# Optimization experiments

Hardware: AMD Instinct MI355X
Metric: run time of the kernel (lower is better)

The kernel has to match this reference:

```python
import jax, jax.numpy as jnp
import numpy as np

B, T, D = 4, 2048, 1024
H = 16
HD = D // H
NORM = float(np.sqrt(D))  # module uses sqrt(out_features), not sqrt(head_dim)


def setup_inputs() -> dict:
    key = jax.random.key(0)
    k1, k2, k3 = jax.random.split(key, 3)
    x = jax.random.normal(k1, (B, T, D), dtype=jnp.float32)
    w_qkv = jax.random.normal(k2, (D, 3 * D), dtype=jnp.float32) * (1.0 / np.sqrt(D))
    w_proj = jax.random.normal(k3, (D, D), dtype=jnp.float32) * (1.0 / np.sqrt(D))
    return {"x": x, "w_qkv": w_qkv, "w_proj": w_proj}


def reference(x, w_qkv, w_proj):
    b, t, _ = x.shape
    qkv = jnp.einsum('btd,de->bte', x, w_qkv)  # [B,T,3D]
    q, k, v = jnp.split(qkv, 3, axis=-1)
    # [B,H,T,HD]
    q = q.reshape(b, t, H, HD).transpose(0, 2, 1, 3)
    k = k.reshape(b, t, H, HD).transpose(0, 2, 1, 3)
    v = v.reshape(b, t, H, HD).transpose(0, 2, 1, 3)
    attn = jnp.einsum('bhqd,bhkd->bhqk', q, k) / NORM
    causal = jnp.tril(jnp.ones((t, t), dtype=bool))
    attn = jnp.where(causal[None, None], attn, -jnp.inf)
    attn = jax.nn.softmax(attn, axis=-1)
    y = jnp.einsum('bhqk,bhkd->bhqd', attn, v)
    out = y.transpose(0, 2, 1, 3).reshape(b, t, D)
    return jnp.einsum('btd,de->bte', out, w_proj)
```

## Files before the change

### kernel.cpp

```cpp
#include <hip/hip_runtime.h>
#include <hip/hip_bf16.h>
#include <cstdint>
#include <cstddef>

typedef __bf16 bfx8 __attribute__((ext_vector_type(8)));
typedef float  fx4  __attribute__((ext_vector_type(4)));
typedef float  fx16 __attribute__((ext_vector_type(16)));

#define MFMA_B16(a, b, c)  __builtin_amdgcn_mfma_f32_16x16x32_bf16((a), (b), (c), 0, 0, 0)
#define MFMA32(a, b, c)    __builtin_amdgcn_mfma_f32_32x32x16_bf16((a), (b), (c), 0, 0, 0)

#define GLD_LDS16(gsrc, ldst)                                                  \
  __builtin_amdgcn_global_load_lds(                                            \
      (const __attribute__((address_space(1))) void*)(gsrc),                   \
      (__attribute__((address_space(3))) void*)(ldst), 16, 0, 0)

static __device__ __forceinline__ unsigned short f2bf(float f) {
  union { float f; unsigned u; } v; v.f = f;
  unsigned r = v.u + 0x7fffu + ((v.u >> 16) & 1u);
  return (unsigned short)(r >> 16);
}

static __device__ __forceinline__ bfx8 ldb8(const unsigned short* p) {
  return *(const bfx8*)(const void*)p;
}

static __device__ __forceinline__ unsigned pk2(float lo, float hi) {
  __hip_bfloat162 h2 = __float22bfloat162_rn(make_float2(lo, hi));
  union { __hip_bfloat162 h; unsigned u; } c; c.h = h2; return c.u;
}

static __device__ __forceinline__ bfx8 scale8(bfx8 x, float s) {
  union { bfx8 v; unsigned u[4]; } a; a.v = x;
  union { bfx8 v; unsigned u[4]; } r;
#pragma unroll
  for (int j = 0; j < 4; ++j) {
    union { unsigned u; float f; } lo, hi;
    lo.u = a.u[j] << 16;
    hi.u = a.u[j] & 0xffff0000u;
    r.u[j] = pk2(lo.f * s, hi.f * s);
  }
  return r.v;
}

#define BB 4
#define TT 2048
#define DD 1024
#define HH 16
#define HD 64

__global__ void k_cast(const float* __restrict__ in, unsigned short* __restrict__ out, int n) {
  int i = (blockIdx.x * blockDim.x + threadIdx.x) * 4;
  int stride = gridDim.x * blockDim.x * 4;
  for (; i < n; i += stride) {
    float4 v = *(const float4*)(in + i);
    ushort4 o;
    o.x = f2bf(v.x); o.y = f2bf(v.y); o.z = f2bf(v.z); o.w = f2bf(v.w);
    *(ushort4*)(out + i) = o;
  }
}

__global__ void k_transpose(const float* __restrict__ in, unsigned short* __restrict__ out,
                            int R, int C) {
  __shared__ float tile[32][33];
  int c0 = blockIdx.x * 32, r0 = blockIdx.y * 32;
  int tx = threadIdx.x, ty = threadIdx.y;
#pragma unroll
  for (int dy = 0; dy < 32; dy += 8)
    tile[ty + dy][tx] = in[(size_t)(r0 + ty + dy) * C + (c0 + tx)];
  __syncthreads();
#pragma unroll
  for (int dy = 0; dy < 32; dy += 8)
    out[(size_t)(c0 + ty + dy) * R + (r0 + tx)] = f2bf(tile[tx][ty + dy]);
}

template <int EPI>
__global__ __launch_bounds__(256) void k_gemm(
    const unsigned short* __restrict__ A,
    const unsigned short* __restrict__ Bt,
    float* __restrict__ outf,
    int M, int N, int K,
    unsigned short* __restrict__ qb, unsigned short* __restrict__ kb,
    unsigned short* __restrict__ vtb) {
  constexpr int BM = 128, BN = 128, BK = 32;
  __shared__ __align__(16) unsigned short As[BM * BK];
  __shared__ __align__(16) unsigned short Bs[BN * BK];

  const int tid  = threadIdx.x;
  const int lane = tid & 63;
  const int w    = tid >> 6;
  const int wr   = w >> 1, wc = w & 1;
  const int n16  = lane & 15, g = lane >> 4;
  const int m0 = blockIdx.y * BM, n0 = blockIdx.x * BN;

  fx4 acc[4][4] = {};

  for (int k0 = 0; k0 < K; k0 += BK) {
#pragma unroll
    for (int iss = 0; iss < 2; ++iss) {
      int bo   = iss * 4096 + w * 1024 + lane * 16;
      int row  = bo >> 6;
      int colb = bo & 63;
      const char* srcA = (const char*)A  + ((size_t)(m0 + row) * K + k0) * 2 + colb;
      const char* srcB = (const char*)Bt + ((size_t)(n0 + row) * K + k0) * 2 + colb;
      GLD_LDS16(srcA, (char*)As + iss * 4096 + w * 1024);
      GLD_LDS16(srcB, (char*)Bs + iss * 4096 + w * 1024);
    }
    __syncthreads();

    bfx8 af[4], bf[4];
#pragma unroll
    for (int mi = 0; mi < 4; ++mi)
      af[mi] = *(const bfx8*)(const void*)&As[(wr * 64 + mi * 16 + n16) * BK + g * 8];
#pragma unroll
    for (int ni = 0; ni < 4; ++ni)
      bf[ni] = *(const bfx8*)(const void*)&Bs[(wc * 64 + ni * 16 + n16) * BK + g * 8];
#pragma unroll
    for (int mi = 0; mi < 4; ++mi)
#pragma unroll
      for (int ni = 0; ni < 4; ++ni)
        acc[mi][ni] = MFMA_B16(af[mi], bf[ni], acc[mi][ni]);
    __syncthreads();
  }

#pragma unroll
  for (int mi = 0; mi < 4; ++mi) {
#pragma unroll
    for (int ni = 0; ni < 4; ++ni) {
      int mrow = m0 + wr * 64 + mi * 16 + g * 4;
      int ncol = n0 + wc * 64 + ni * 16 + n16;
      if (EPI == 0) {
#pragma unroll
        for (int i = 0; i < 4; ++i)
          outf[(size_t)(mrow + i) * N + ncol] = acc[mi][ni][i];
      } else {
        int sec = ncol >> 10;
        int h   = (ncol >> 6) & 15;
        int d   = ncol & 63;
#pragma unroll
        for (int i = 0; i < 4; ++i) {
          int mm = mrow + i;
          int b  = mm >> 11;
          int t  = mm & 2047;
          unsigned short val = f2bf(acc[mi][ni][i]);
          if (sec == 0)
            qb[(((size_t)(b * HH + h) * TT + t) << 6) + d] = val;
          else if (sec == 1)
            kb[(((size_t)(b * HH + h) * TT + t) << 6) + d] = val;
          else
            vtb[((size_t)(b * HH + h) * HD + d) * TT + t] = val;
        }
      }
    }
  }
}

struct KVfrag { bfx8 k0, k1, k2, k3, v0, v1, v2, v3; };

static __device__ __forceinline__ void load_kv(
    KVfrag& f, const unsigned short* __restrict__ kbase,
    const unsigned short* __restrict__ vbase, int kv0) {
  const unsigned short* kr = kbase + (size_t)kv0 * HD;
  f.k0 = ldb8(kr);       f.k1 = ldb8(kr + 16);
  f.k2 = ldb8(kr + 32);  f.k3 = ldb8(kr + 48);
  const unsigned short* vr = vbase + kv0;
  f.v0 = ldb8(vr);            f.v1 = ldb8(vr + 16);
  f.v2 = ldb8(vr + 32 * TT);  f.v3 = ldb8(vr + 32 * TT + 16);
}

static __device__ __forceinline__ void attn_tile(
    const KVfrag& f, const bfx8* qf, int lim, int hi,
    float& m, float& l, fx16& o0, fx16& o1) {
  fx16 s = {};
  s = MFMA32(f.k0, qf[0], s);
  s = MFMA32(f.k1, qf[1], s);
  s = MFMA32(f.k2, qf[2], s);
  s = MFMA32(f.k3, qf[3], s);

  float t[16];
#pragma unroll
  for (int r = 0; r < 16; ++r) {
    int koff = (r & 3) + 8 * (r >> 2);
    t[r] = (koff <= lim) ? s[r] : -__builtin_inff();
  }
  float x0 = fmaxf(t[0], t[1]),   x1 = fmaxf(t[2], t[3]);
  float x2 = fmaxf(t[4], t[5]),   x3 = fmaxf(t[6], t[7]);
  float x4 = fmaxf(t[8], t[9]),   x5 = fmaxf(t[10], t[11]);
  float x6 = fmaxf(t[12], t[13]), x7 = fmaxf(t[14], t[15]);
  float y0 = fmaxf(x0, x1), y1 = fmaxf(x2, x3), y2 = fmaxf(x4, x5), y3 = fmaxf(x6, x7);
  float mx = fmaxf(fmaxf(y0, y1), fmaxf(y2, y3));

  bool need = mx > m + 8.0f;
  if (__ballot(need) != 0ull) {
    float mo   = fmaxf(mx, __shfl_xor(mx, 32));
    float mnew = fmaxf(m, mo);
    float alpha = __builtin_amdgcn_exp2f(m - mnew);
    m = mnew;
    l *= alpha;
#pragma unroll
    for (int r = 0; r < 16; ++r) { o0[r] *= alpha; o1[r] *= alpha; }
  }

  float p[16];
#pragma unroll
  for (int r = 0; r < 16; ++r) p[r] = __builtin_amdgcn_exp2f(t[r] - m);
  float s0 = (p[0] + p[1]) + (p[2] + p[3]);
  float s1 = (p[4] + p[5]) + (p[6] + p[7]);
  float s2 = (p[8] + p[9]) + (p[10] + p[11]);
  float s3 = (p[12] + p[13]) + (p[14] + p[15]);
  l += (s0 + s1) + (s2 + s3);

  union { unsigned u[4]; bfx8 v; } P0, P1;
#pragma unroll
  for (int c = 0; c < 2; ++c) {
    unsigned a0 = pk2(p[8*c+0], p[8*c+1]);
    unsigned a1 = pk2(p[8*c+2], p[8*c+3]);
    unsigned b0 = pk2(p[8*c+4], p[8*c+5]);
    unsigned b1 = pk2(p[8*c+6], p[8*c+7]);
    unsigned xa0 = __shfl_xor(a0, 32), xa1 = __shfl_xor(a1, 32);
    unsigned xb0 = __shfl_xor(b0, 32), xb1 = __shfl_xor(b1, 32);
    unsigned* U = c ? P1.u : P0.u;
    U[0] = hi ? xb0 : a0;
    U[1] = hi ? xb1 : a1;
    U[2] = hi ? b0 : xa0;
    U[3] = hi ? b1 : xa1;
  }
  o0 = MFMA32(f.v0, P0.v, o0);
  o0 = MFMA32(f.v1, P1.v, o0);
  o1 = MFMA32(f.v2, P0.v, o1);
  o1 = MFMA32(f.v3, P1.v, o1);
}

static __device__ __forceinline__ void run_qtile(
    int i, const unsigned short* __restrict__ qbb,
    const unsigned short* __restrict__ kbase,
    const unsigned short* __restrict__ vbase,
    unsigned short* __restrict__ ybase0,
    int l31, int hi) {
  const int q0 = i * 32;
  const float CL = 0.0450842346f;
  const unsigned short* qp = qbb + (size_t)(q0 + l31) * HD + hi * 8;
  bfx8 qf[4];
#pragma unroll
  for (int dc = 0; dc < 4; ++dc) qf[dc] = scale8(ldb8(qp + dc * 16), CL);

  fx16 o0 = {}, o1 = {};
  float m = -__builtin_inff(), l = 0.f;
  const int nt   = i + 1;
  const int limd = l31 - 4 * hi;
  const int BIG  = 127;

  KVfrag A, B, C;
  load_kv(A, kbase, vbase, 0);
  load_kv(B, kbase, vbase, nt > 1 ? 32 : 0);

  int t = 0;
  for (; t + 3 < nt; t += 3) {
    load_kv(C, kbase, vbase, (t + 2) * 32);
    attn_tile(A, qf, BIG, hi, m, l, o0, o1);
    load_kv(A, kbase, vbase, (t + 3) * 32);
    attn_tile(B, qf, BIG, hi, m, l, o0, o1);
    int nx = (t + 4 < nt) ? (t + 4) : (nt - 1);
    load_kv(B, kbase, vbase, nx * 32);
    attn_tile(C, qf, BIG, hi, m, l, o0, o1);
  }
  {
    const int r = nt - t;
    if (r == 3) load_kv(C, kbase, vbase, (t + 2) * 32);
    attn_tile(A, qf, (r == 1) ? limd : BIG, hi, m, l, o0, o1);
    if (r >= 2) attn_tile(B, qf, (r == 2) ? limd : BIG, hi, m, l, o0, o1);
    if (r == 3) attn_tile(C, qf, limd, hi, m, l, o0, o1);
  }

  l += __shfl_xor(l, 32);
  float inv = 1.0f / l;
  unsigned short* yp = ybase0 + (size_t)(q0 + l31) * DD + 4 * hi;
#pragma unroll
  for (int g = 0; g < 4; ++g) {
    ushort4 s4;
    s4.x = f2bf(o0[4*g+0] * inv); s4.y = f2bf(o0[4*g+1] * inv);
    s4.z = f2bf(o0[4*g+2] * inv); s4.w = f2bf(o0[4*g+3] * inv);
    *(ushort4*)(yp + 8 * g) = s4;
    s4.x = f2bf(o1[4*g+0] * inv); s4.y = f2bf(o1[4*g+1] * inv);
    s4.z = f2bf(o1[4*g+2] * inv); s4.w = f2bf(o1[4*g+3] * inv);
    *(ushort4*)(yp + 32 + 8 * g) = s4;
  }
}

__global__ __launch_bounds__(256) void k_attn(
    const unsigned short* __restrict__ qb,
    const unsigned short* __restrict__ kb,
    const unsigned short* __restrict__ vtb,
    unsigned short* __restrict__ yb) {
  const int tid  = threadIdx.x;
  const int lane = tid & 63;
  const int w    = tid >> 6;
  const int l31  = lane & 31;
  const int hi   = lane >> 5;

  int blk = blockIdx.x;
  int j  = blk & 7;
  int h  = (blk >> 3) & 15;
  int b  = blk >> 7;
  const int i = j * 4 + w;
  const size_t bh = (size_t)b * HH + h;

  const unsigned short* qbb   = qb  + bh * TT * HD;
  const unsigned short* kbase = kb  + bh * TT * HD + (size_t)l31 * HD + hi * 8;
  const unsigned short* vbase = vtb + (bh * HD + l31) * TT + hi * 8;
  unsigned short* ybase0      = yb  + (size_t)b * TT * DD + h * HD;

  run_qtile(i,      qbb, kbase, vbase, ybase0, l31, hi);
  run_qtile(63 - i, qbb, kbase, vbase, ybase0, l31, hi);
}

extern "C" void kernel_launch(void* const* d_in, const int* in_sizes, int n_in,
                              void* d_out, int out_size, void* d_ws, size_t ws_size,
                              hipStream_t stream) {
  const float* x      = (const float*)d_in[0];
  const float* w_qkv  = (const float*)d_in[1];
  const float* w_proj = (const float*)d_in[2];
  float* out = (float*)d_out;

  char* ws = (char*)d_ws;
  unsigned short* xb     = (unsigned short*)(ws);
  unsigned short* wqkvT  = (unsigned short*)(ws + (size_t)(16u << 20));
  unsigned short* wprojT = (unsigned short*)(ws + (size_t)(22u << 20));
  unsigned short* qb     = (unsigned short*)(ws + (size_t)(24u << 20));
  unsigned short* kb     = (unsigned short*)(ws + (size_t)(40u << 20));
  unsigned short* vtb    = (unsigned short*)(ws + (size_t)(56u << 20));
  unsigned short* yb     = xb;

  k_cast<<<4096, 256, 0, stream>>>(x, xb, BB * TT * DD);

  dim3 tb(32, 8);
  k_transpose<<<dim3(3 * DD / 32, DD / 32), tb, 0, stream>>>(w_qkv, wqkvT, DD, 3 * DD);
  k_transpose<<<dim3(DD / 32, DD / 32), tb, 0, stream>>>(w_proj, wprojT, DD, DD);

  k_gemm<1><<<dim3(3 * DD / 128, BB * TT / 128), 256, 0, stream>>>(
      xb, wqkvT, nullptr, BB * TT, 3 * DD, DD, qb, kb, vtb);

  k_attn<<<BB * HH * 8, 256, 0, stream>>>(qb, kb, vtb, yb);

  k_gemm<0><<<dim3(DD / 128, BB * TT / 128), 256, 0, stream>>>(
      yb, wprojT, out, BB * TT, DD, DD, nullptr, nullptr, nullptr);
}
```

Before: 263.8 us.

## Share K/V tiles across waves via double-buffered swizzled LDS staging in attention

The attention kernel now stages 64-row K and V^T chunks into double-buffered, XOR-swizzled LDS with global_load_lds, so 8 waves handling 8 consecutive 32-row query tiles share each load. Previously every wave streamed its own K/V fragments from global memory directly into registers. Each block now covers a contiguous 256-query strip, which drops the old balanced pairing (i, 63-i), so the causal work per block becomes uneven, and a __syncthreads is added per chunk.

```diff
diff --git a/kernel.cpp b/kernel.cpp
--- a/kernel.cpp
+++ b/kernel.cpp
@@ -21,8 +21,8 @@
   return (unsigned short)(r >> 16);
 }
 
-static __device__ __forceinline__ bfx8 ldb8(const unsigned short* p) {
-  return *(const bfx8*)(const void*)p;
+static __device__ __forceinline__ bfx8 ldb8(const void* p) {
+  return *(const bfx8*)p;
 }
 
 static __device__ __forceinline__ unsigned pk2(float lo, float hi) {
@@ -155,27 +155,40 @@
   }
 }
 
-struct KVfrag { bfx8 k0, k1, k2, k3, v0, v1, v2, v3; };
-
-static __device__ __forceinline__ void load_kv(
-    KVfrag& f, const unsigned short* __restrict__ kbase,
-    const unsigned short* __restrict__ vbase, int kv0) {
-  const unsigned short* kr = kbase + (size_t)kv0 * HD;
-  f.k0 = ldb8(kr);       f.k1 = ldb8(kr + 16);
-  f.k2 = ldb8(kr + 32);  f.k3 = ldb8(kr + 48);
-  const unsigned short* vr = vbase + kv0;
-  f.v0 = ldb8(vr);            f.v1 = ldb8(vr + 16);
-  f.v2 = ldb8(vr + 32 * TT);  f.v3 = ldb8(vr + 32 * TT + 16);
-}
-
-static __device__ __forceinline__ void attn_tile(
-    const KVfrag& f, const bfx8* qf, int lim, int hi,
+
+static __device__ __forceinline__ void stage64(
+    const char* __restrict__ kbb, const char* __restrict__ vbb, size_t kv0,
+    char* ldsK, char* ldsV, int w, int lane) {
+  int dest = w * 1024 + lane * 16;
+  int row  = dest >> 7;
+  int colb = dest & 127;
+  int scol = colb ^ ((row & 7) << 4);
+  GLD_LDS16(kbb + (kv0 + row) * 128 + scol, ldsK + w * 1024);
+  GLD_LDS16(vbb + (size_t)row * (TT * 2) + kv0 * 2 + scol, ldsV + w * 1024);
+}
+
+static __device__ __forceinline__ void attn_tile_lds(
+    const char* __restrict__ kbuf, const char* __restrict__ vbuf, int tt,
+    const bfx8* qf, int lim, int hi, int l31,
     float& m, float& l, fx16& o0, fx16& o1) {
+  const int r7 = (l31 & 7) << 4;
+  const char* krow = kbuf + (size_t)(tt * 32 + l31) * 128;
+  bfx8 kf0 = ldb8(krow + ((hi * 16 +  0) ^ r7));
+  bfx8 kf1 = ldb8(krow + ((hi * 16 + 32) ^ r7));
+  bfx8 kf2 = ldb8(krow + ((hi * 16 + 64) ^ r7));
+  bfx8 kf3 = ldb8(krow + ((hi * 16 + 96) ^ r7));
+  const char* vrow0 = vbuf + (size_t)l31 * 128;
+  const char* vrow1 = vbuf + (size_t)(l31 + 32) * 128;
+  const int c0 = (tt * 64 + hi * 16) ^ r7;
+  const int c1 = (tt * 64 + 32 + hi * 16) ^ r7;
+  bfx8 vf0 = ldb8(vrow0 + c0), vf1 = ldb8(vrow0 + c1);
+  bfx8 vf2 = ldb8(vrow1 + c0), vf3 = ldb8(vrow1 + c1);
+
   fx16 s = {};
-  s = MFMA32(f.k0, qf[0], s);
-  s = MFMA32(f.k1, qf[1], s);
-  s = MFMA32(f.k2, qf[2], s);
-  s = MFMA32(f.k3, qf[3], s);
+  s = MFMA32(kf0, qf[0], s);
+  s = MFMA32(kf1, qf[1], s);
+  s = MFMA32(kf2, qf[2], s);
+  s = MFMA32(kf3, qf[3], s);
 
   float t[16];
 #pragma unroll
@@ -225,56 +238,72 @@
     U[2] = hi ? b0 : xa0;
     U[3] = hi ? b1 : xa1;
   }
-  o0 = MFMA32(f.v0, P0.v, o0);
-  o0 = MFMA32(f.v1, P1.v, o0);
-  o1 = MFMA32(f.v2, P0.v, o1);
-  o1 = MFMA32(f.v3, P1.v, o1);
-}
-
-static __device__ __forceinline__ void run_qtile(
-    int i, const unsigned short* __restrict__ qbb,
-    const unsigned short* __restrict__ kbase,
-    const unsigned short* __restrict__ vbase,
-    unsigned short* __restrict__ ybase0,
-    int l31, int hi) {
-  const int q0 = i * 32;
+  o0 = MFMA32(vf0, P0.v, o0);
+  o0 = MFMA32(vf1, P1.v, o0);
+  o1 = MFMA32(vf2, P0.v, o1);
+  o1 = MFMA32(vf3, P1.v, o1);
+}
+
+__global__ __launch_bounds__(512) void k_attn(
+    const unsigned short* __restrict__ qb,
+    const unsigned short* __restrict__ kb,
+    const unsigned short* __restrict__ vtb,
+    unsigned short* __restrict__ yb) {
+  __shared__ __align__(16) unsigned short Ks[2][4096];
+  __shared__ __align__(16) unsigned short Vs[2][4096];
+
+  const int tid  = threadIdx.x;
+  const int lane = tid & 63;
+  const int w    = tid >> 6;
+  const int l31  = lane & 31;
+  const int hi   = lane >> 5;
+
+  int blk = blockIdx.x;
+  const int s = 7 - (blk & 7);
+  const int h = (blk >> 3) & 15;
+  const int b = blk >> 7;
+  const size_t bh = (size_t)b * HH + h;
+
+  const int qw = s * 256 + w * 32;
+  const int NC = 4 * (s + 1);
+
+  const char* kbb = (const char*)(kb + bh * TT * HD);
+  const char* vbb = (const char*)(vtb + bh * HD * TT);
+
   const float CL = 0.0450842346f;
-  const unsigned short* qp = qbb + (size_t)(q0 + l31) * HD + hi * 8;
+  const unsigned short* qp = qb + (bh * TT + qw + l31) * HD + hi * 8;
   bfx8 qf[4];
 #pragma unroll
   for (int dc = 0; dc < 4; ++dc) qf[dc] = scale8(ldb8(qp + dc * 16), CL);
 
   fx16 o0 = {}, o1 = {};
   float m = -__builtin_inff(), l = 0.f;
-  const int nt   = i + 1;
   const int limd = l31 - 4 * hi;
   const int BIG  = 127;
 
-  KVfrag A, B, C;
-  load_kv(A, kbase, vbase, 0);
-  load_kv(B, kbase, vbase, nt > 1 ? 32 : 0);
-
-  int t = 0;
-  for (; t + 3 < nt; t += 3) {
-    load_kv(C, kbase, vbase, (t + 2) * 32);
-    attn_tile(A, qf, BIG, hi, m, l, o0, o1);
-    load_kv(A, kbase, vbase, (t + 3) * 32);
-    attn_tile(B, qf, BIG, hi, m, l, o0, o1);
-    int nx = (t + 4 < nt) ? (t + 4) : (nt - 1);
-    load_kv(B, kbase, vbase, nx * 32);
-    attn_tile(C, qf, BIG, hi, m, l, o0, o1);
-  }
-  {
-    const int r = nt - t;
-    if (r == 3) load_kv(C, kbase, vbase, (t + 2) * 32);
-    attn_tile(A, qf, (r == 1) ? limd : BIG, hi, m, l, o0, o1);
-    if (r >= 2) attn_tile(B, qf, (r == 2) ? limd : BIG, hi, m, l, o0, o1);
-    if (r == 3) attn_tile(C, qf, limd, hi, m, l, o0, o1);
+  stage64(kbb, vbb, 0, (char*)Ks[0], (char*)Vs[0], w, lane);
+  __syncthreads();
+
+  int cur = 0;
+#pragma unroll 1
+  for (int c = 0; c < NC; ++c) {
+    if (c + 1 < NC)
+      stage64(kbb, vbb, (size_t)(c + 1) * 64,
+              (char*)Ks[cur ^ 1], (char*)Vs[cur ^ 1], w, lane);
+    const char* kbuf = (const char*)Ks[cur];
+    const char* vbuf = (const char*)Vs[cur];
+    const int kv0 = c * 64;
+    if (kv0 <= qw)
+      attn_tile_lds(kbuf, vbuf, 0, qf, (kv0 == qw) ? limd : BIG, hi, l31, m, l, o0, o1);
+    if (kv0 + 32 <= qw)
+      attn_tile_lds(kbuf, vbuf, 1, qf, (kv0 + 32 == qw) ? limd : BIG, hi, l31, m, l, o0, o1);
+    __syncthreads();
+    cur ^= 1;
   }
 
   l += __shfl_xor(l, 32);
   float inv = 1.0f / l;
-  unsigned short* yp = ybase0 + (size_t)(q0 + l31) * DD + 4 * hi;
+  unsigned short* yp = yb + (size_t)(b * TT + qw + l31) * DD + h * HD + 4 * hi;
 #pragma unroll
   for (int g = 0; g < 4; ++g) {
     ushort4 s4;
@@ -287,33 +316,6 @@
   }
 }
 
-__global__ __launch_bounds__(256) void k_attn(
-    const unsigned short* __restrict__ qb,
-    const unsigned short* __restrict__ kb,
-    const unsigned short* __restrict__ vtb,
-    unsigned short* __restrict__ yb) {
-  const int tid  = threadIdx.x;
-  const int lane = tid & 63;
-  const int w    = tid >> 6;
-  const int l31  = lane & 31;
-  const int hi   = lane >> 5;
-
-  int blk = blockIdx.x;
-  int j  = blk & 7;
-  int h  = (blk >> 3) & 15;
-  int b  = blk >> 7;
-  const int i = j * 4 + w;
-  const size_t bh = (size_t)b * HH + h;
-
-  const unsigned short* qbb   = qb  + bh * TT * HD;
-  const unsigned short* kbase = kb  + bh * TT * HD + (size_t)l31 * HD + hi * 8;
-  const unsigned short* vbase = vtb + (bh * HD + l31) * TT + hi * 8;
-  unsigned short* ybase0      = yb  + (size_t)b * TT * DD + h * HD;
-
-  run_qtile(i,      qbb, kbase, vbase, ybase0, l31, hi);
-  run_qtile(63 - i, qbb, kbase, vbase, ybase0, l31, hi);
-}
-
 extern "C" void kernel_launch(void* const* d_in, const int* in_sizes, int n_in,
                               void* d_out, int out_size, void* d_ws, size_t ws_size,
                               hipStream_t stream) {
@@ -340,7 +342,7 @@
   k_gemm<1><<<dim3(3 * DD / 128, BB * TT / 128), 256, 0, stream>>>(
       xb, wqkvT, nullptr, BB * TT, 3 * DD, DD, qb, kb, vtb);
 
-  k_attn<<<BB * HH * 8, 256, 0, stream>>>(qb, kb, vtb, yb);
+  k_attn<<<BB * HH * 8, 512, 0, stream>>>(qb, kb, vtb, yb);
 
   k_gemm<0><<<dim3(DD / 128, BB * TT / 128), 256, 0, stream>>>(
       yb, wprojT, out, BB * TT, DD, DD, nullptr, nullptr, nullptr);
```

Measured after the change: 291.4 us. 10.5% more time.
